# Optimization experiments

Hardware: AMD Instinct MI355X
Metric: run time of the kernel (lower is better)

Reference implementation:

```python
import jax, jax.numpy as jnp
import numpy as np

N_NODES = 50000
N_EDGES = 800000
D_IN = 64
D_OUT = 64


def setup_inputs() -> dict:
    key = jax.random.key(0)
    k = jax.random.split(key, 5)
    stdv = 1.0 / np.sqrt(D_OUT)
    X = jax.random.normal(k[0], (N_NODES, D_IN), jnp.float32)
    weights = jax.random.uniform(k[1], (D_IN, D_OUT), jnp.float32, -stdv, stdv)
    attention_w = jax.random.normal(k[2], (1, 1), jnp.float32)
    # edge list: row = destination (segment) ids, sorted (CSR-like); col = source ids
    row = jnp.sort(jax.random.randint(k[3], (N_EDGES,), 0, N_NODES, jnp.int32))
    col = jax.random.randint(k[4], (N_EDGES,), 0, N_NODES, jnp.int32)
    return {"X": X, "weights": weights, "attention_w": attention_w, "row": row, "col": col}


def reference(X, weights, attention_w, row, col):
    # dense linear
    Xp = X @ weights  # [N, D_OUT]
    # SDDMM: per-edge dot product between dst and src transformed features
    edge_feature = jnp.einsum('ed,ed->e', Xp[row], Xp[col])  # [E]
    # scale by scalar attention weight (n_heads = 1)
    edge_attn = edge_feature * attention_w[0, 0]  # [E]
    # SpMM aggregation: out[i] = sum_{e: row[e]=i} edge_attn[e] * Xp[col[e]]
    out = jax.ops.segment_sum(edge_attn[:, None] * Xp[col], row,
                              num_segments=X.shape[0])  # [N, D_OUT]
    return out
```

## Files before the change

kernel.cpp:

```cpp
#include <hip/hip_runtime.h>
#include <hip/hip_bf16.h>

#define D 64

__device__ __forceinline__ void bf16x8_to_f32(uint4 u, float f[8]) {
    union { unsigned int i; float x; } t;
    t.i = u.x << 16;          f[0] = t.x;
    t.i = u.x & 0xFFFF0000u;  f[1] = t.x;
    t.i = u.y << 16;          f[2] = t.x;
    t.i = u.y & 0xFFFF0000u;  f[3] = t.x;
    t.i = u.z << 16;          f[4] = t.x;
    t.i = u.z & 0xFFFF0000u;  f[5] = t.x;
    t.i = u.w << 16;          f[6] = t.x;
    t.i = u.w & 0xFFFF0000u;  f[7] = t.x;
}

__global__ __launch_bounds__(256) void gemm_kernel(const float* __restrict__ X,
                                                   const float* __restrict__ W,
                                                   __hip_bfloat16* __restrict__ Xp,
                                                   int nNodes) {
    int lane = threadIdx.x & 63;
    int wave = (blockIdx.x * 256 + threadIdx.x) >> 6;
    int nWaves = gridDim.x * 4;

    float w[D];
#pragma unroll
    for (int k = 0; k < D; ++k) w[k] = W[k * D + lane];

    for (int r = wave; r < nNodes; r += nWaves) {
        int row = __builtin_amdgcn_readfirstlane(r);
        const float4* xr = (const float4*)(X + (size_t)row * D);
        float acc = 0.f;
#pragma unroll
        for (int k4 = 0; k4 < D / 4; ++k4) {
            float4 xv = xr[k4];
            acc = fmaf(xv.x, w[4 * k4 + 0], acc);
            acc = fmaf(xv.y, w[4 * k4 + 1], acc);
            acc = fmaf(xv.z, w[4 * k4 + 2], acc);
            acc = fmaf(xv.w, w[4 * k4 + 3], acc);
        }
        Xp[(size_t)row * D + lane] = __float2bfloat16(acc);
    }
}

__global__ __launch_bounds__(256) void rowptr_kernel(const int* __restrict__ row,
                                                     int* __restrict__ rowptr,
                                                     int nNodes, int nEdges) {
    int e = blockIdx.x * 256 + threadIdx.x;
    if (e >= nEdges) return;
    int r = row[e];
    int rprev = (e == 0) ? -1 : row[e - 1];
    for (int q = rprev + 1; q <= r; ++q) rowptr[q] = e;
    if (e == nEdges - 1) {
        for (int q = r + 1; q <= nNodes; ++q) rowptr[q] = nEdges;
    }
}

__global__ __launch_bounds__(256) void fused_kernel(const __hip_bfloat16* __restrict__ Xp,
                                                    const int* __restrict__ rowptr,
                                                    const int* __restrict__ col,
                                                    const float* __restrict__ attn_w,
                                                    float* __restrict__ out,
                                                    int nNodes) {
    int lane = threadIdx.x & 63;
    int node = (blockIdx.x * 256 + threadIdx.x) >> 6;
    if (node >= nNodes) return;
    int g = lane >> 3;
    int j = lane & 7;

    int eStart = rowptr[node];
    int eEnd   = rowptr[node + 1];
    float attn = attn_w[0];

    const uint4* XpV = (const uint4*)Xp;
    float xr[8];
    bf16x8_to_f32(XpV[(size_t)node * 8 + j], xr);

    float acc[8] = {0.f, 0.f, 0.f, 0.f, 0.f, 0.f, 0.f, 0.f};

    for (int cb = eStart; cb < eEnd; cb += 64) {
        int myE = cb + lane;
        int cidx = (myE < eEnd) ? col[myE] : -1;
        int nrem = eEnd - cb;

#pragma unroll
        for (int m = 0; m < 4; ++m) {
            if (16 * m >= nrem) break;
            int c0 = __shfl(cidx, 16 * m + g, 64);
            int c1 = __shfl(cidx, 16 * m + 8 + g, 64);
            bool v0 = c0 >= 0, v1 = c1 >= 0;
            uint4 u0 = XpV[(size_t)(v0 ? c0 : 0) * 8 + j];
            uint4 u1 = XpV[(size_t)(v1 ? c1 : 0) * 8 + j];
            float x0[8], x1[8];
            bf16x8_to_f32(u0, x0);
            bf16x8_to_f32(u1, x1);

            float p0 = 0.f, p1 = 0.f;
#pragma unroll
            for (int q = 0; q < 8; ++q) { p0 = fmaf(xr[q], x0[q], p0);
                                          p1 = fmaf(xr[q], x1[q], p1); }
#pragma unroll
            for (int off = 1; off < 8; off <<= 1) { p0 += __shfl_xor(p0, off, 64);
                                                    p1 += __shfl_xor(p1, off, 64); }
            float s0 = v0 ? p0 * attn : 0.f;
            float s1 = v1 ? p1 * attn : 0.f;
#pragma unroll
            for (int q = 0; q < 8; ++q) { acc[q] = fmaf(s0, x0[q], acc[q]);
                                          acc[q] = fmaf(s1, x1[q], acc[q]); }
        }
    }

#pragma unroll
    for (int off = 8; off < 64; off <<= 1)
#pragma unroll
        for (int q = 0; q < 8; ++q) acc[q] += __shfl_xor(acc[q], off, 64);

    if (g == 0) {
        float4* o = (float4*)(out + (size_t)node * D + 8 * j);
        o[0] = make_float4(acc[0], acc[1], acc[2], acc[3]);
        o[1] = make_float4(acc[4], acc[5], acc[6], acc[7]);
    }
}

extern "C" void kernel_launch(void* const* d_in, const int* in_sizes, int n_in,
                              void* d_out, int out_size, void* d_ws, size_t ws_size,
                              hipStream_t stream) {
    const float* X    = (const float*)d_in[0];
    const float* W    = (const float*)d_in[1];
    const float* attn = (const float*)d_in[2];
    const int*   row  = (const int*)d_in[3];
    const int*   col  = (const int*)d_in[4];
    float* out = (float*)d_out;

    int nNodes = in_sizes[0] / D;
    int nEdges = in_sizes[3];

    __hip_bfloat16* Xp = (__hip_bfloat16*)d_ws;
    int* rowptr = (int*)((char*)d_ws + (size_t)nNodes * D * sizeof(__hip_bfloat16));

    gemm_kernel<<<1024, 256, 0, stream>>>(X, W, Xp, nNodes);
    rowptr_kernel<<<(nEdges + 255) / 256, 256, 0, stream>>>(row, rowptr, nNodes, nEdges);
    fused_kernel<<<(nNodes + 3) / 4, 256, 0, stream>>>(Xp, rowptr, col, attn, out, nNodes);
}
```

Before: 115.6 us.

## Map eight nodes per wave, merge GEMM and rowptr kernels, store Xp as fp16

The aggregation kernel now gives each 8-lane group its own destination node, so one wave handles eight nodes instead of one. Each group walks that node's edges four at a time, loading the column indices directly and removing the cross-group reduction at the end. The GEMM and rowptr construction are fused into a single launch using a block-index split, and the intermediate Xp is stored as fp16 instead of bf16. The per-group mapping risks load imbalance between groups within a wave and issues more serial, dependent col loads per group. Storing fp16 also changes the precision and range of the intermediate.

```diff
diff --git a/kernel.cpp b/kernel.cpp
--- a/kernel.cpp
+++ b/kernel.cpp
@@ -1,35 +1,45 @@
 #include <hip/hip_runtime.h>
-#include <hip/hip_bf16.h>
+#include <hip/hip_fp16.h>
 
 #define D 64
 
-__device__ __forceinline__ void bf16x8_to_f32(uint4 u, float f[8]) {
-    union { unsigned int i; float x; } t;
-    t.i = u.x << 16;          f[0] = t.x;
-    t.i = u.x & 0xFFFF0000u;  f[1] = t.x;
-    t.i = u.y << 16;          f[2] = t.x;
-    t.i = u.y & 0xFFFF0000u;  f[3] = t.x;
-    t.i = u.z << 16;          f[4] = t.x;
-    t.i = u.z & 0xFFFF0000u;  f[5] = t.x;
-    t.i = u.w << 16;          f[6] = t.x;
-    t.i = u.w & 0xFFFF0000u;  f[7] = t.x;
+__device__ __forceinline__ void h8_to_f32(uint4 u, float f[8]) {
+    float2 t;
+    t = __half22float2(*(const __half2*)&u.x); f[0] = t.x; f[1] = t.y;
+    t = __half22float2(*(const __half2*)&u.y); f[2] = t.x; f[3] = t.y;
+    t = __half22float2(*(const __half2*)&u.z); f[4] = t.x; f[5] = t.y;
+    t = __half22float2(*(const __half2*)&u.w); f[6] = t.x; f[7] = t.y;
 }
 
-__global__ __launch_bounds__(256) void gemm_kernel(const float* __restrict__ X,
+__global__ __launch_bounds__(256) void prep_kernel(const float* __restrict__ X,
                                                    const float* __restrict__ W,
-                                                   __hip_bfloat16* __restrict__ Xp,
-                                                   int nNodes) {
+                                                   const int* __restrict__ row,
+                                                   __half* __restrict__ Xp,
+                                                   int* __restrict__ rowptr,
+                                                   int nNodes, int nEdges,
+                                                   int gemmBlocks) {
+    if ((int)blockIdx.x >= gemmBlocks) {
+        int e = (blockIdx.x - gemmBlocks) * 256 + threadIdx.x;
+        if (e >= nEdges) return;
+        int r = row[e];
+        int rprev = (e == 0) ? -1 : row[e - 1];
+        for (int q = rprev + 1; q <= r; ++q) rowptr[q] = e;
+        if (e == nEdges - 1) {
+            for (int q = r + 1; q <= nNodes; ++q) rowptr[q] = nEdges;
+        }
+        return;
+    }
     int lane = threadIdx.x & 63;
     int wave = (blockIdx.x * 256 + threadIdx.x) >> 6;
-    int nWaves = gridDim.x * 4;
+    int nWaves = gemmBlocks * 4;
 
     float w[D];
 #pragma unroll
     for (int k = 0; k < D; ++k) w[k] = W[k * D + lane];
 
     for (int r = wave; r < nNodes; r += nWaves) {
-        int row = __builtin_amdgcn_readfirstlane(r);
-        const float4* xr = (const float4*)(X + (size_t)row * D);
+        int rr = __builtin_amdgcn_readfirstlane(r);
+        const float4* xr = (const float4*)(X + (size_t)rr * D);
         float acc = 0.f;
 #pragma unroll
         for (int k4 = 0; k4 < D / 4; ++k4) {
@@ -39,83 +49,73 @@
             acc = fmaf(xv.z, w[4 * k4 + 2], acc);
             acc = fmaf(xv.w, w[4 * k4 + 3], acc);
         }
-        Xp[(size_t)row * D + lane] = __float2bfloat16(acc);
+        Xp[(size_t)rr * D + lane] = __float2half(acc);
     }
 }
 
-__global__ __launch_bounds__(256) void rowptr_kernel(const int* __restrict__ row,
-                                                     int* __restrict__ rowptr,
-                                                     int nNodes, int nEdges) {
-    int e = blockIdx.x * 256 + threadIdx.x;
-    if (e >= nEdges) return;
-    int r = row[e];
-    int rprev = (e == 0) ? -1 : row[e - 1];
-    for (int q = rprev + 1; q <= r; ++q) rowptr[q] = e;
-    if (e == nEdges - 1) {
-        for (int q = r + 1; q <= nNodes; ++q) rowptr[q] = nEdges;
-    }
-}
-
-__global__ __launch_bounds__(256) void fused_kernel(const __hip_bfloat16* __restrict__ Xp,
+__global__ __launch_bounds__(256) void fused_kernel(const __half* __restrict__ Xp,
                                                     const int* __restrict__ rowptr,
                                                     const int* __restrict__ col,
                                                     const float* __restrict__ attn_w,
                                                     float* __restrict__ out,
                                                     int nNodes) {
     int lane = threadIdx.x & 63;
-    int node = (blockIdx.x * 256 + threadIdx.x) >> 6;
-    if (node >= nNodes) return;
+    int waveId = (blockIdx.x * 256 + threadIdx.x) >> 6;
     int g = lane >> 3;
     int j = lane & 7;
 
-    int eStart = rowptr[node];
-    int eEnd   = rowptr[node + 1];
+    int node = waveId * 8 + g;
+    bool active = node < nNodes;
+    int nd = active ? node : (nNodes - 1);
+
+    int eStart = rowptr[nd];
+    int eEnd   = active ? rowptr[nd + 1] : eStart;
     float attn = attn_w[0];
 
     const uint4* XpV = (const uint4*)Xp;
     float xr[8];
-    bf16x8_to_f32(XpV[(size_t)node * 8 + j], xr);
+    h8_to_f32(XpV[(size_t)nd * 8 + j], xr);
 
     float acc[8] = {0.f, 0.f, 0.f, 0.f, 0.f, 0.f, 0.f, 0.f};
 
-    for (int cb = eStart; cb < eEnd; cb += 64) {
-        int myE = cb + lane;
-        int cidx = (myE < eEnd) ? col[myE] : -1;
-        int nrem = eEnd - cb;
+    for (int e = eStart; e < eEnd; e += 4) {
+        bool v[4];
+        int  c[4];
+#pragma unroll
+        for (int u = 0; u < 4; ++u) {
+            int ee = e + u;
+            v[u] = ee < eEnd;
+            c[u] = col[v[u] ? ee : eStart];
+        }
+        uint4 raw[4];
+#pragma unroll
+        for (int u = 0; u < 4; ++u)
+            raw[u] = XpV[(size_t)c[u] * 8 + j];
 
+        float xf[4][8];
+        float p[4];
 #pragma unroll
-        for (int m = 0; m < 4; ++m) {
-            if (16 * m >= nrem) break;
-            int c0 = __shfl(cidx, 16 * m + g, 64);
-            int c1 = __shfl(cidx, 16 * m + 8 + g, 64);
-            bool v0 = c0 >= 0, v1 = c1 >= 0;
-            uint4 u0 = XpV[(size_t)(v0 ? c0 : 0) * 8 + j];
-            uint4 u1 = XpV[(size_t)(v1 ? c1 : 0) * 8 + j];
-            float x0[8], x1[8];
-            bf16x8_to_f32(u0, x0);
-            bf16x8_to_f32(u1, x1);
-
-            float p0 = 0.f, p1 = 0.f;
+        for (int u = 0; u < 4; ++u) {
+            h8_to_f32(raw[u], xf[u]);
+            float s = 0.f;
 #pragma unroll
-            for (int q = 0; q < 8; ++q) { p0 = fmaf(xr[q], x0[q], p0);
-                                          p1 = fmaf(xr[q], x1[q], p1); }
+            for (int q = 0; q < 8; ++q) s = fmaf(xr[q], xf[u][q], s);
+            p[u] = s;
+        }
 #pragma unroll
-            for (int off = 1; off < 8; off <<= 1) { p0 += __shfl_xor(p0, off, 64);
-                                                    p1 += __shfl_xor(p1, off, 64); }
-            float s0 = v0 ? p0 * attn : 0.f;
-            float s1 = v1 ? p1 * attn : 0.f;
+        for (int off = 1; off < 8; off <<= 1) {
 #pragma unroll
-            for (int q = 0; q < 8; ++q) { acc[q] = fmaf(s0, x0[q], acc[q]);
-                                          acc[q] = fmaf(s1, x1[q], acc[q]); }
+            for (int u = 0; u < 4; ++u) p[u] += __shfl_xor(p[u], off, 64);
+        }
+#pragma unroll
+        for (int u = 0; u < 4; ++u) {
+            float s = v[u] ? p[u] * attn : 0.f;
+#pragma unroll
+            for (int q = 0; q < 8; ++q) acc[q] = fmaf(s, xf[u][q], acc[q]);
         }
     }
 
-#pragma unroll
-    for (int off = 8; off < 64; off <<= 1)
-#pragma unroll
-        for (int q = 0; q < 8; ++q) acc[q] += __shfl_xor(acc[q], off, 64);
-
-    if (g == 0) {
+    if (active) {
         float4* o = (float4*)(out + (size_t)node * D + 8 * j);
         o[0] = make_float4(acc[0], acc[1], acc[2], acc[3]);
         o[1] = make_float4(acc[4], acc[5], acc[6], acc[7]);
@@ -135,10 +135,14 @@
     int nNodes = in_sizes[0] / D;
     int nEdges = in_sizes[3];
 
-    __hip_bfloat16* Xp = (__hip_bfloat16*)d_ws;
-    int* rowptr = (int*)((char*)d_ws + (size_t)nNodes * D * sizeof(__hip_bfloat16));
+    __half* Xp  = (__half*)d_ws;
+    int* rowptr = (int*)((char*)d_ws + (size_t)nNodes * D * sizeof(__half));
 
-    gemm_kernel<<<1024, 256, 0, stream>>>(X, W, Xp, nNodes);
-    rowptr_kernel<<<(nEdges + 255) / 256, 256, 0, stream>>>(row, rowptr, nNodes, nEdges);
-    fused_kernel<<<(nNodes + 3) / 4, 256, 0, stream>>>(Xp, rowptr, col, attn, out, nNodes);
+    int gemmBlocks = 1024;
+    int rpBlocks   = (nEdges + 255) / 256;
+    prep_kernel<<<gemmBlocks + rpBlocks, 256, 0, stream>>>(X, W, row, Xp, rowptr,
+                                                           nNodes, nEdges, gemmBlocks);
+
+    int waves = (nNodes + 7) / 8;
+    fused_kernel<<<(waves + 3) / 4, 256, 0, stream>>>(Xp, rowptr, col, attn, out, nNodes);
 }
```

After: 106.2 us. -8.1%, faster.
